# Optimization experiments

Hardware: AMD Instinct MI355X
Metric: run time of the kernel (lower is better)

Reference implementation:

```python
import jax, jax.numpy as jnp
import numpy as np

VOL = 100.0  # cubic volume (100,100,100)


def _forward(x, positions, input_weights, features, output_weights,
             connection_radii, thresholds, n_iterations):
    # clamp positions into the volume (per-axis, min 0.1, max VOL-0.1)
    pos = jnp.clip(positions, 0.1, VOL - 0.1)                      # [N,3]
    radii = jnp.clip(connection_radii, 1.0, 50.0)                  # [N]
    # pairwise Euclidean distances via ||a||^2 + ||b||^2 - 2ab (avoids [N,N,3])
    sq = jnp.sum(pos * pos, axis=1)
    d2 = jnp.maximum(sq[:, None] + sq[None, :] - 2.0 * (pos @ pos.T), 0.0)
    pos_mask = d2 > 0.0
    dist = jnp.where(pos_mask, jnp.sqrt(jnp.where(pos_mask, d2, 1.0)), 0.0)  # [N,N]
    max_r = jnp.max(radii)
    conn_mask = (dist < max_r).astype(dist.dtype)
    atten = jnp.exp(-jnp.minimum(dist / (radii[:, None] + 1e-6), 20.0)) * conn_mask
    # feature similarity (F.normalize uses eps as a clamp-min on the norm)
    fn = features / jnp.maximum(jnp.linalg.norm(features, axis=1, keepdims=True), 1e-6)
    feat_sim = fn @ fn.T                                            # [N,N]
    cw = atten * (0.3 + 0.7 * jnp.clip(feat_sim, -1.0, 1.0))
    cw = cw / (jnp.sum(cw, axis=1, keepdims=True) + 1e-6)           # row-normalized [N,N]
    # spatial input / output gating along x-axis
    xc = jnp.clip(pos[:, 0] / VOL, 0.0, 1.0)                        # [N]
    iw = jnp.exp(-3.0 * xc)
    iw = iw / (jnp.sum(iw) + 1e-6)
    act = (x @ input_weights.T) * iw                                # [B,N]
    for _ in range(n_iterations):
        act = jnp.minimum(jax.nn.relu(act + act @ cw.T - thresholds), 100.0)
    ow = jnp.exp(3.0 * (xc - 1.0))
    ow = ow / (jnp.sum(ow) + 1e-6)
    return (act * ow) @ output_weights                              # [B,out]


def setup_inputs() -> dict:
    key = jax.random.key(0)
    ks = jax.random.split(key, 5)
    N, IN, OUT, FD, B = 8000, 784, 10, 32, 64
    return {
        "x": jax.random.normal(ks[0], (B, IN), jnp.float32),
        "positions": jax.random.uniform(ks[1], (N, 3), jnp.float32) * VOL,
        "input_weights": jax.random.normal(ks[2], (N, IN), jnp.float32) * 0.01,
        "features": jax.random.normal(ks[3], (N, FD), jnp.float32) * 0.1,
        "output_weights": jax.random.normal(ks[4], (N, OUT), jnp.float32) * 0.01,
        "connection_radii": jnp.ones((N,), jnp.float32) * 15.0,
        "thresholds": jnp.zeros((N,), jnp.float32),
        "n_iterations": 2,
    }


def reference(x, positions, input_weights, features, output_weights,
              connection_radii, thresholds, n_iterations):
    return _forward(x, positions, input_weights, features, output_weights,
                    connection_radii, thresholds, n_iterations)
```

## Files before the change

### kernel.cpp

```cpp
#include <hip/hip_runtime.h>
#include <hip/hip_bf16.h>
#include <math.h>

#define VOLF 100.0f
#define FD 32
#define OUT_DIM 10
#define MAXN 320
#define MAX_LAUNCH_ITERS 4
#define KSPLIT 7
#define BM 64
#define BKQ 28
#define SRW 2
#define SRB 8
#define OB 128

__global__ __launch_bounds__(256) void k_pre(
    const float* __restrict__ positions, const float* __restrict__ radii_in,
    const float* __restrict__ features, float* __restrict__ posx4,
    float* __restrict__ radii, float* __restrict__ e_iw, float* __restrict__ e_ow,
    float* __restrict__ fn, float* __restrict__ scal, int N)
{
    int i = blockIdx.x * blockDim.x + threadIdx.x;
    float my_iw = 0.0f, my_ow = 0.0f, my_r = 0.0f;
    if (i < N) {
        float px = fminf(fmaxf(positions[3*i+0], 0.1f), VOLF - 0.1f);
        float py = fminf(fmaxf(positions[3*i+1], 0.1f), VOLF - 0.1f);
        float pz = fminf(fmaxf(positions[3*i+2], 0.1f), VOLF - 0.1f);
        float sq = px*px + py*py + pz*pz;
        posx4[4*i+0] = px; posx4[4*i+1] = py; posx4[4*i+2] = pz; posx4[4*i+3] = sq;
        float r = fminf(fmaxf(radii_in[i], 1.0f), 50.0f);
        radii[i] = r; my_r = r;
        float xc = fminf(fmaxf(px / VOLF, 0.0f), 1.0f);
        my_iw = expf(-3.0f * xc);
        my_ow = expf(3.0f * (xc - 1.0f));
        e_iw[i] = my_iw; e_ow[i] = my_ow;
        float s = 0.0f;
        #pragma unroll
        for (int k = 0; k < FD; k++) { float v = features[(size_t)i*FD + k]; s += v*v; }
        float nrm = fmaxf(sqrtf(s), 1e-6f);
        #pragma unroll
        for (int k = 0; k < FD; k++) fn[(size_t)i*FD + k] = features[(size_t)i*FD + k] / nrm;
    }
    __shared__ float red[256];
    red[threadIdx.x] = my_iw; __syncthreads();
    for (int s = 128; s > 0; s >>= 1) { if (threadIdx.x < s) red[threadIdx.x] += red[threadIdx.x + s]; __syncthreads(); }
    if (threadIdx.x == 0) atomicAdd(&scal[0], red[0]);
    __syncthreads();
    red[threadIdx.x] = my_ow; __syncthreads();
    for (int s = 128; s > 0; s >>= 1) { if (threadIdx.x < s) red[threadIdx.x] += red[threadIdx.x + s]; __syncthreads(); }
    if (threadIdx.x == 0) atomicAdd(&scal[1], red[0]);
    if (i < N) atomicMax((int*)&scal[2], __float_as_int(my_r));
}

__global__ __launch_bounds__(256) void k_xt(const float* __restrict__ x, float* __restrict__ xT,
                                            int B, int IN)
{
    int idx = blockIdx.x * blockDim.x + threadIdx.x;
    if (idx < B * IN) {
        int b = idx / IN, k = idx % IN;
        xT[(size_t)k * B + b] = x[idx];
    }
}

__global__ __launch_bounds__(256) void k_act0(
    const float* __restrict__ xT, const float* __restrict__ Wi,
    float* __restrict__ partial, int N, int IN)
{
    __shared__ float4 xs4[BKQ * 64];
    __shared__ float  wt[BM * 112];
    int t = threadIdx.x;
    int i0 = blockIdx.x * BM;
    int k0 = blockIdx.y * 112;
    #pragma unroll
    for (int fi = t; fi < BM * 28; fi += 256) {
        int row = fi / 28, cq = fi % 28;
        ((float4*)wt)[row * 28 + cq] = *(const float4*)(Wi + (size_t)(i0 + row) * IN + k0 + cq * 4);
    }
    {
        int l = t & 63, q = t >> 6;
        #pragma unroll
        for (int kq = q; kq < BKQ; kq += 4) {
            float4 v;
            v.x = xT[(size_t)(k0 + 4*kq + 0) * 64 + l];
            v.y = xT[(size_t)(k0 + 4*kq + 1) * 64 + l];
            v.z = xT[(size_t)(k0 + 4*kq + 2) * 64 + l];
            v.w = xT[(size_t)(k0 + 4*kq + 3) * 64 + l];
            xs4[kq * 64 + l] = v;
        }
    }
    __syncthreads();
    int wave = t >> 6, lane = t & 63;
    int nbase = wave * 16;
    float acc[16];
    #pragma unroll
    for (int n = 0; n < 16; n++) acc[n] = 0.0f;
    for (int kq = 0; kq < BKQ; kq++) {
        float4 xv = xs4[kq * 64 + lane];
        #pragma unroll
        for (int n = 0; n < 16; n++) {
            float4 w = ((const float4*)(wt + (nbase + n) * 112))[kq];
            acc[n] += w.x * xv.x + w.y * xv.y + w.z * xv.z + w.w * xv.w;
        }
    }
    size_t base = ((size_t)blockIdx.y * N + (i0 + nbase)) * 64 + lane;
    #pragma unroll
    for (int n = 0; n < 16; n++)
        partial[base + (size_t)n * 64] = acc[n];
}

__global__ __launch_bounds__(256) void k_act0_red(
    const float* __restrict__ partial, const float* __restrict__ e_iw,
    const float* __restrict__ scal, float* __restrict__ actA, int N)
{
    int idx = blockIdx.x * 256 + threadIdx.x;
    int i = idx >> 6;
    size_t stride = (size_t)N * 64;
    float s = 0.0f;
    #pragma unroll
    for (int ks = 0; ks < KSPLIT; ks++) s += partial[ks * stride + idx];
    float inv = 1.0f / (scal[0] + 1e-6f);
    actA[idx] = s * (e_iw[i] * inv);
}

__device__ __forceinline__ void scan_body(
    const float4& p, const float4& q, int j, float maxr,
    unsigned long long lmask, int2* __restrict__ ep, size_t base, int& cnt)
{
    float d2 = fmaxf(p.w + q.w - 2.0f*(p.x*q.x + p.y*q.y + p.z*q.z), 0.0f);
    float dist = sqrtf(d2);
    bool hit = dist < maxr;
    unsigned long long m = __ballot(hit);
    if (m) {
        if (hit) {
            int pos = cnt + (int)__popcll(m & lmask);
            if (pos < MAXN) ep[base + pos] = make_int2(j, __float_as_int(dist));
        }
        cnt += (int)__popcll(m);
    }
}

__global__ __launch_bounds__(256) void k_scan(
    const float* __restrict__ posx4, const float* __restrict__ scal,
    int2* __restrict__ ep, int* __restrict__ nbr_cnt, int N)
{
    int wave = threadIdx.x >> 6, lane = threadIdx.x & 63;
    int r0 = blockIdx.x * SRB + wave * SRW;
    float4 p0 = ((const float4*)posx4)[r0];
    float4 p1 = ((const float4*)posx4)[r0 + 1];
    float maxr = __int_as_float(((const int*)scal)[2]);
    unsigned long long lmask = (1ull << lane) - 1ull;
    int c0 = 0, c1 = 0;
    size_t base0 = (size_t)r0 * MAXN, base1 = base0 + MAXN;
    int jb = 0;
    for (; jb + 128 <= N; jb += 128) {
        int j0 = jb + lane, j1 = jb + 64 + lane;
        float4 q0 = ((const float4*)posx4)[j0];
        float4 q1 = ((const float4*)posx4)[j1];
        scan_body(p0, q0, j0, maxr, lmask, ep, base0, c0);
        scan_body(p1, q0, j0, maxr, lmask, ep, base1, c1);
        scan_body(p0, q1, j1, maxr, lmask, ep, base0, c0);
        scan_body(p1, q1, j1, maxr, lmask, ep, base1, c1);
    }
    for (; jb < N; jb += 64) {
        int j0 = jb + lane;
        float4 q0 = ((const float4*)posx4)[j0];
        scan_body(p0, q0, j0, maxr, lmask, ep, base0, c0);
        scan_body(p1, q0, j0, maxr, lmask, ep, base1, c1);
    }
    if (lane == 0) {
        nbr_cnt[r0]     = min(c0, MAXN);
        nbr_cnt[r0 + 1] = min(c1, MAXN);
    }
}

__global__ __launch_bounds__(256) void k_weight(
    const float* __restrict__ fn, const float* __restrict__ radii,
    int2* __restrict__ ep ,
    const int* __restrict__ nbr_cnt, float* __restrict__ rowinv, int N)
{
    int i = blockIdx.x;
    int lane = threadIdx.x & 63;
    int wave = threadIdx.x >> 6;
    int sub = lane & 7;
    int eg  = lane >> 3;
    float4 fni = ((const float4*)(fn + (size_t)i * FD))[sub];
    float inv_ri = 1.0f / (radii[i] + 1e-6f);
    int cnt = nbr_cnt[i];
    float s = 0.0f;
    for (int e0 = wave * 8; e0 < cnt; e0 += 32) {
        int e = e0 + eg;
        bool act = e < cnt;
        int ecl = act ? e : (cnt - 1);
        int2 edge = ep[(size_t)i * MAXN + ecl];
        int j      = edge.x;
        float dist = __int_as_float(edge.y);
        float4 fj = ((const float4*)(fn + (size_t)j * FD))[sub];
        float fs = fni.x*fj.x + fni.y*fj.y + fni.z*fj.z + fni.w*fj.w;
        fs += __shfl_xor(fs, 1, 64);
        fs += __shfl_xor(fs, 2, 64);
        fs += __shfl_xor(fs, 4, 64);
        fs = fminf(fmaxf(fs, -1.0f), 1.0f);
        float w = expf(-fminf(dist * inv_ri, 20.0f)) * (0.3f + 0.7f * fs);
        if (act && sub == 0) {
            ((float*)&ep[(size_t)i * MAXN + e])[1] = w;
            s += w;
        }
    }
    __shared__ float red[256];
    red[threadIdx.x] = s; __syncthreads();
    for (int st = 128; st > 0; st >>= 1) { if (threadIdx.x < st) red[threadIdx.x] += red[threadIdx.x + st]; __syncthreads(); }
    if (threadIdx.x == 0) rowinv[i] = 1.0f / (red[0] + 1e-6f);
}

__global__ __launch_bounds__(256) void k_iter(
    const float* __restrict__ actIn, float* __restrict__ actOut,
    const int2* __restrict__ ep, const int* __restrict__ nbr_cnt,
    const float* __restrict__ rowinv, const float* __restrict__ thr,
    const int* __restrict__ nIterPtr, int iterIdx, int N)
{
    if (iterIdx >= min(*nIterPtr, MAX_LAUNCH_ITERS)) return;
    int i = blockIdx.x;
    int wave = threadIdx.x >> 6, lane = threadIdx.x & 63;
    int cnt = nbr_cnt[i];
    float acc = 0.0f;
    for (int e = wave; e < cnt; e += 4) {
        int2 edge = ep[(size_t)i * MAXN + e];
        acc += actIn[(size_t)edge.x * 64 + lane] * __int_as_float(edge.y);
    }
    __shared__ float redA[4 * 64];
    redA[wave * 64 + lane] = acc;
    __syncthreads();
    if (wave == 0) {
        float tot = redA[lane] + redA[64 + lane] + redA[128 + lane] + redA[192 + lane];
        float v = actIn[(size_t)i * 64 + lane] + tot * rowinv[i] - thr[i];
        v = fminf(fmaxf(v, 0.0f), 100.0f);
        actOut[(size_t)i * 64 + lane] = v;
    }
}

__global__ __launch_bounds__(256) void k_out1(
    const float* __restrict__ actA, const float* __restrict__ actB,
    const int* __restrict__ nIterPtr, const float* __restrict__ e_ow,
    const float* __restrict__ scal, const float* __restrict__ outW,
    float* __restrict__ outPart, int N)
{
    int m = min(*nIterPtr, MAX_LAUNCH_ITERS);
    const float* actF = (m & 1) ? actB : actA;
    int wave = threadIdx.x >> 6, lane = threadIdx.x & 63;
    float inv = 1.0f / (scal[1] + 1e-6f);
    float acc[OUT_DIM];
    #pragma unroll
    for (int o = 0; o < OUT_DIM; o++) acc[o] = 0.0f;
    for (int i = blockIdx.x * 4 + wave; i < N; i += OB * 4) {
        float a = actF[(size_t)i * 64 + lane] * (e_ow[i] * inv);
        const float* wo = outW + (size_t)i * OUT_DIM;
        #pragma unroll
        for (int o = 0; o < OUT_DIM; o++) acc[o] += a * wo[o];
    }
    __shared__ float red[4][OUT_DIM][64];
    #pragma unroll
    for (int o = 0; o < OUT_DIM; o++) red[wave][o][lane] = acc[o];
    __syncthreads();
    if (wave == 0) {
        #pragma unroll
        for (int o = 0; o < OUT_DIM; o++) {
            float s = red[0][o][lane] + red[1][o][lane] + red[2][o][lane] + red[3][o][lane];
            outPart[((size_t)blockIdx.x * OUT_DIM + o) * 64 + lane] = s;
        }
    }
}

__global__ __launch_bounds__(256) void k_out2(
    const float* __restrict__ outPart, float* __restrict__ out)
{
    int t = blockIdx.x * 256 + threadIdx.x;
    if (t >= 64 * OUT_DIM) return;
    int b = t / OUT_DIM, o = t % OUT_DIM;
    float s = 0.0f;
    for (int blk = 0; blk < OB; blk++)
        s += outPart[((size_t)blk * OUT_DIM + o) * 64 + b];
    out[t] = s;
}

extern "C" void kernel_launch(void* const* d_in, const int* in_sizes, int n_in,
                              void* d_out, int out_size, void* d_ws, size_t ws_size,
                              hipStream_t stream)
{
    const float* x        = (const float*)d_in[0];
    const float* positions= (const float*)d_in[1];
    const float* Win      = (const float*)d_in[2];
    const float* features = (const float*)d_in[3];
    const float* Wout     = (const float*)d_in[4];
    const float* radii_in = (const float*)d_in[5];
    const float* thr      = (const float*)d_in[6];
    const int*   nIter    = (const int*)  d_in[7];

    const int N  = in_sizes[5];
    const int IN = in_sizes[2] / N;
    const int B  = in_sizes[0] / IN;
    (void)B;

    float* ws = (float*)d_ws;
    size_t off = 0;
    auto alloc = [&](size_t nfloats) { size_t cur = off; off += (nfloats + 63) & ~(size_t)63; return cur; };
    float* xT      = ws + alloc((size_t)B * IN);
    float* posx4   = ws + alloc((size_t)N * 4);
    float* radii   = ws + alloc(N);
    float* e_iw    = ws + alloc(N);
    float* e_ow    = ws + alloc(N);
    float* rowinv  = ws + alloc(N);
    float* scal    = ws + alloc(4);
    float* outPart = ws + alloc((size_t)OB * OUT_DIM * 64);
    float* fn      = ws + alloc((size_t)N * FD);
    float* actA    = ws + alloc((size_t)N * 64);
    float* actB    = ws + alloc((size_t)N * 64);
    int2*  ep      = (int2*)(ws + alloc((size_t)N * MAXN * 2));
    int*   nbr_cnt = (int*)(ws + alloc(N));
    float* partial = (float*)ep;

    hipMemsetAsync(scal, 0, 4 * sizeof(float), stream);

    k_pre<<<(N + 255) / 256, 256, 0, stream>>>(positions, radii_in, features,
                                               posx4, radii, e_iw, e_ow, fn, scal, N);
    k_xt<<<(B * IN + 255) / 256, 256, 0, stream>>>(x, xT, B, IN);
    k_act0<<<dim3(N / BM, KSPLIT), 256, 0, stream>>>(xT, Win, partial, N, IN);
    k_act0_red<<<(N * 64) / 256, 256, 0, stream>>>(partial, e_iw, scal, actA, N);
    k_scan<<<N / SRB, 256, 0, stream>>>(posx4, scal, ep, nbr_cnt, N);
    k_weight<<<N, 256, 0, stream>>>(fn, radii, ep, nbr_cnt, rowinv, N);

    float* bufs[2] = {actA, actB};
    for (int it = 0; it < MAX_LAUNCH_ITERS; it++) {
        k_iter<<<N, 256, 0, stream>>>(bufs[it & 1], bufs[(it + 1) & 1],
                                      ep, nbr_cnt, rowinv, thr, nIter, it, N);
    }
    k_out1<<<OB, 256, 0, stream>>>(actA, actB, nIter, e_ow, scal, Wout, outPart, N);
    k_out2<<<3, 256, 0, stream>>>(outPart, (float*)d_out);
}
```

Measured before the change: 254.4 us.

## Fuse prep kernels, fold edge weighting into scan, retile input GEMM

Merges the x-transpose kernel into the preprocessing kernel, and folds the per-row edge weighting and row-sum into the neighbour-scan kernel so one wave handles its rows end to end. The input projection GEMM is retiled into a register-blocked outer product (4x16 per thread) with a transposed weight tile in shared memory, K split into 4 blocks and intra-block wave pairs reduced before writing 8 partial slices. This cuts launch count and redundant ep/fn traffic, but leaves fewer threads for the weighting step and adds more partial-sum slices to reduce.

```diff
diff --git a/kernel.cpp b/kernel.cpp
--- a/kernel.cpp
+++ b/kernel.cpp
@@ -7,20 +7,30 @@
 #define OUT_DIM 10
 #define MAXN 320
 #define MAX_LAUNCH_ITERS 4
-#define KSPLIT 7
-#define BM 64
-#define BKQ 28
 #define SRW 2
 #define SRB 8
 #define OB 128
-
-__global__ __launch_bounds__(256) void k_pre(
-    const float* __restrict__ positions, const float* __restrict__ radii_in,
-    const float* __restrict__ features, float* __restrict__ posx4,
+#define CHUNK 28
+#define NCHUNK 7
+#define LDP 68
+#define PS 8
+
+__global__ __launch_bounds__(256) void k_prext(
+    const float* __restrict__ x, const float* __restrict__ positions,
+    const float* __restrict__ radii_in, const float* __restrict__ features,
+    float* __restrict__ xT, float* __restrict__ posx4,
     float* __restrict__ radii, float* __restrict__ e_iw, float* __restrict__ e_ow,
-    float* __restrict__ fn, float* __restrict__ scal, int N)
-{
-    int i = blockIdx.x * blockDim.x + threadIdx.x;
+    float* __restrict__ fn, float* __restrict__ scal, int N, int B, int IN, int nxt)
+{
+    if ((int)blockIdx.x < nxt) {
+        int idx = blockIdx.x * 256 + threadIdx.x;
+        if (idx < B * IN) {
+            int b = idx / IN, k = idx % IN;
+            xT[(size_t)k * B + b] = x[idx];
+        }
+        return;
+    }
+    int i = (blockIdx.x - nxt) * 256 + threadIdx.x;
     float my_iw = 0.0f, my_ow = 0.0f, my_r = 0.0f;
     if (i < N) {
         float px = fminf(fmaxf(positions[3*i+0], 0.1f), VOLF - 0.1f);
@@ -52,60 +62,81 @@
     if (i < N) atomicMax((int*)&scal[2], __float_as_int(my_r));
 }
 
-__global__ __launch_bounds__(256) void k_xt(const float* __restrict__ x, float* __restrict__ xT,
-                                            int B, int IN)
-{
-    int idx = blockIdx.x * blockDim.x + threadIdx.x;
-    if (idx < B * IN) {
-        int b = idx / IN, k = idx % IN;
-        xT[(size_t)k * B + b] = x[idx];
-    }
-}
-
 __global__ __launch_bounds__(256) void k_act0(
     const float* __restrict__ xT, const float* __restrict__ Wi,
     float* __restrict__ partial, int N, int IN)
 {
-    __shared__ float4 xs4[BKQ * 64];
-    __shared__ float  wt[BM * 112];
+    __shared__ float smem[2 * 64 * 68];
+    float* wtT = smem;
     int t = threadIdx.x;
-    int i0 = blockIdx.x * BM;
-    int k0 = blockIdx.y * 112;
-    #pragma unroll
-    for (int fi = t; fi < BM * 28; fi += 256) {
-        int row = fi / 28, cq = fi % 28;
-        ((float4*)wt)[row * 28 + cq] = *(const float4*)(Wi + (size_t)(i0 + row) * IN + k0 + cq * 4);
-    }
-    {
-        int l = t & 63, q = t >> 6;
-        #pragma unroll
-        for (int kq = q; kq < BKQ; kq += 4) {
-            float4 v;
-            v.x = xT[(size_t)(k0 + 4*kq + 0) * 64 + l];
-            v.y = xT[(size_t)(k0 + 4*kq + 1) * 64 + l];
-            v.z = xT[(size_t)(k0 + 4*kq + 2) * 64 + l];
-            v.w = xT[(size_t)(k0 + 4*kq + 3) * 64 + l];
-            xs4[kq * 64 + l] = v;
-        }
-    }
-    __syncthreads();
     int wave = t >> 6, lane = t & 63;
-    int nbase = wave * 16;
-    float acc[16];
-    #pragma unroll
-    for (int n = 0; n < 16; n++) acc[n] = 0.0f;
-    for (int kq = 0; kq < BKQ; kq++) {
-        float4 xv = xs4[kq * 64 + lane];
-        #pragma unroll
-        for (int n = 0; n < 16; n++) {
-            float4 w = ((const float4*)(wt + (nbase + n) * 112))[kq];
-            acc[n] += w.x * xv.x + w.y * xv.y + w.z * xv.z + w.w * xv.w;
-        }
-    }
-    size_t base = ((size_t)blockIdx.y * N + (i0 + nbase)) * 64 + lane;
-    #pragma unroll
-    for (int n = 0; n < 16; n++)
-        partial[base + (size_t)n * 64] = acc[n];
+    int nr = lane >> 2, br = lane & 3;
+    int i0 = blockIdx.x * 64;
+    int kbase = blockIdx.y * 196;
+    float acc[4][16];
+    #pragma unroll
+    for (int a = 0; a < 4; a++)
+        #pragma unroll
+        for (int b = 0; b < 16; b++) acc[a][b] = 0.0f;
+
+    for (int c = 0; c < NCHUNK; c++) {
+        int k0 = kbase + c * CHUNK;
+        __syncthreads();
+        for (int fi = t; fi < 64 * (CHUNK/4); fi += 256) {
+            int n = fi / (CHUNK/4), q = fi % (CHUNK/4);
+            float4 w4 = *(const float4*)(Wi + (size_t)(i0 + n) * IN + k0 + q * 4);
+            wtT[(q*4+0)*LDP + n] = w4.x;
+            wtT[(q*4+1)*LDP + n] = w4.y;
+            wtT[(q*4+2)*LDP + n] = w4.z;
+            wtT[(q*4+3)*LDP + n] = w4.w;
+        }
+        __syncthreads();
+        for (int q = ((wave + c) & 3); q < CHUNK/4; q += 4) {
+            #pragma unroll
+            for (int j = 0; j < 4; j++) {
+                int kl = q*4 + j;
+                float4 a4 = *(const float4*)(&wtT[kl * LDP + nr*4]);
+                const float* xr = xT + (size_t)(k0 + kl) * 64 + br*16;
+                float4 b0 = *(const float4*)(xr + 0);
+                float4 b1 = *(const float4*)(xr + 4);
+                float4 b2 = *(const float4*)(xr + 8);
+                float4 b3 = *(const float4*)(xr + 12);
+                #pragma unroll
+                for (int a = 0; a < 4; a++) {
+                    float av = (a==0) ? a4.x : (a==1) ? a4.y : (a==2) ? a4.z : a4.w;
+                    acc[a][ 0] += av*b0.x; acc[a][ 1] += av*b0.y; acc[a][ 2] += av*b0.z; acc[a][ 3] += av*b0.w;
+                    acc[a][ 4] += av*b1.x; acc[a][ 5] += av*b1.y; acc[a][ 6] += av*b1.z; acc[a][ 7] += av*b1.w;
+                    acc[a][ 8] += av*b2.x; acc[a][ 9] += av*b2.y; acc[a][10] += av*b2.z; acc[a][11] += av*b2.w;
+                    acc[a][12] += av*b3.x; acc[a][13] += av*b3.y; acc[a][14] += av*b3.z; acc[a][15] += av*b3.w;
+                }
+            }
+        }
+    }
+    __syncthreads();
+    float4* sm4 = (float4*)smem;
+    int g = wave >> 1;
+    if (wave & 1) {
+        #pragma unroll
+        for (int a = 0; a < 4; a++)
+            #pragma unroll
+            for (int b4 = 0; b4 < 4; b4++)
+                sm4[(g*16 + a*4 + b4) * 64 + lane] =
+                    make_float4(acc[a][b4*4+0], acc[a][b4*4+1], acc[a][b4*4+2], acc[a][b4*4+3]);
+    }
+    __syncthreads();
+    if (!(wave & 1)) {
+        int slot = blockIdx.y * 2 + g;
+        size_t pbase = ((size_t)slot * N + i0 + nr*4) * 64 + br*16;
+        #pragma unroll
+        for (int a = 0; a < 4; a++)
+            #pragma unroll
+            for (int b4 = 0; b4 < 4; b4++) {
+                float4 o = sm4[(g*16 + a*4 + b4) * 64 + lane];
+                o.x += acc[a][b4*4+0]; o.y += acc[a][b4*4+1];
+                o.z += acc[a][b4*4+2]; o.w += acc[a][b4*4+3];
+                *(float4*)(partial + pbase + (size_t)a * 64 + b4*4) = o;
+            }
+    }
 }
 
 __global__ __launch_bounds__(256) void k_act0_red(
@@ -117,7 +148,7 @@
     size_t stride = (size_t)N * 64;
     float s = 0.0f;
     #pragma unroll
-    for (int ks = 0; ks < KSPLIT; ks++) s += partial[ks * stride + idx];
+    for (int p = 0; p < PS; p++) s += partial[p * stride + idx];
     float inv = 1.0f / (scal[0] + 1e-6f);
     actA[idx] = s * (e_iw[i] * inv);
 }
@@ -141,7 +172,8 @@
 
 __global__ __launch_bounds__(256) void k_scan(
     const float* __restrict__ posx4, const float* __restrict__ scal,
-    int2* __restrict__ ep, int* __restrict__ nbr_cnt, int N)
+    const float* __restrict__ fn, const float* __restrict__ radii,
+    int2* __restrict__ ep, int* __restrict__ nbr_cnt, float* __restrict__ rowinv, int N)
 {
     int wave = threadIdx.x >> 6, lane = threadIdx.x & 63;
     int r0 = blockIdx.x * SRB + wave * SRW;
@@ -171,45 +203,38 @@
         nbr_cnt[r0]     = min(c0, MAXN);
         nbr_cnt[r0 + 1] = min(c1, MAXN);
     }
-}
-
-__global__ __launch_bounds__(256) void k_weight(
-    const float* __restrict__ fn, const float* __restrict__ radii,
-    int2* __restrict__ ep ,
-    const int* __restrict__ nbr_cnt, float* __restrict__ rowinv, int N)
-{
-    int i = blockIdx.x;
-    int lane = threadIdx.x & 63;
-    int wave = threadIdx.x >> 6;
     int sub = lane & 7;
     int eg  = lane >> 3;
-    float4 fni = ((const float4*)(fn + (size_t)i * FD))[sub];
-    float inv_ri = 1.0f / (radii[i] + 1e-6f);
-    int cnt = nbr_cnt[i];
-    float s = 0.0f;
-    for (int e0 = wave * 8; e0 < cnt; e0 += 32) {
-        int e = e0 + eg;
-        bool act = e < cnt;
-        int ecl = act ? e : (cnt - 1);
-        int2 edge = ep[(size_t)i * MAXN + ecl];
-        int j      = edge.x;
-        float dist = __int_as_float(edge.y);
-        float4 fj = ((const float4*)(fn + (size_t)j * FD))[sub];
-        float fs = fni.x*fj.x + fni.y*fj.y + fni.z*fj.z + fni.w*fj.w;
-        fs += __shfl_xor(fs, 1, 64);
-        fs += __shfl_xor(fs, 2, 64);
-        fs += __shfl_xor(fs, 4, 64);
-        fs = fminf(fmaxf(fs, -1.0f), 1.0f);
-        float w = expf(-fminf(dist * inv_ri, 20.0f)) * (0.3f + 0.7f * fs);
-        if (act && sub == 0) {
-            ((float*)&ep[(size_t)i * MAXN + e])[1] = w;
-            s += w;
-        }
-    }
-    __shared__ float red[256];
-    red[threadIdx.x] = s; __syncthreads();
-    for (int st = 128; st > 0; st >>= 1) { if (threadIdx.x < st) red[threadIdx.x] += red[threadIdx.x + st]; __syncthreads(); }
-    if (threadIdx.x == 0) rowinv[i] = 1.0f / (red[0] + 1e-6f);
+    #pragma unroll
+    for (int rr = 0; rr < SRW; rr++) {
+        int r = r0 + rr;
+        int cnt = min(rr == 0 ? c0 : c1, MAXN);
+        size_t base = (size_t)r * MAXN;
+        float4 fni = ((const float4*)(fn + (size_t)r * FD))[sub];
+        float inv_ri = 1.0f / (radii[r] + 1e-6f);
+        float s = 0.0f;
+        for (int e0 = 0; e0 < cnt; e0 += 8) {
+            int e = e0 + eg;
+            bool act = e < cnt;
+            int ecl = act ? e : cnt - 1;
+            int2 edge = ep[base + ecl];
+            float dist = __int_as_float(edge.y);
+            float4 fj = ((const float4*)(fn + (size_t)edge.x * FD))[sub];
+            float fs = fni.x*fj.x + fni.y*fj.y + fni.z*fj.z + fni.w*fj.w;
+            fs += __shfl_xor(fs, 1, 64);
+            fs += __shfl_xor(fs, 2, 64);
+            fs += __shfl_xor(fs, 4, 64);
+            fs = fminf(fmaxf(fs, -1.0f), 1.0f);
+            float w = expf(-fminf(dist * inv_ri, 20.0f)) * (0.3f + 0.7f * fs);
+            if (act && sub == 0) {
+                ((float*)&ep[base + e])[1] = w;
+                s += w;
+            }
+        }
+        s += __shfl_xor(s, 1, 64);  s += __shfl_xor(s, 2, 64);  s += __shfl_xor(s, 4, 64);
+        s += __shfl_xor(s, 8, 64);  s += __shfl_xor(s, 16, 64); s += __shfl_xor(s, 32, 64);
+        if (lane == 0) rowinv[r] = 1.0f / (s + 1e-6f);
+    }
 }
 
 __global__ __launch_bounds__(256) void k_iter(
@@ -298,7 +323,6 @@
     const int N  = in_sizes[5];
     const int IN = in_sizes[2] / N;
     const int B  = in_sizes[0] / IN;
-    (void)B;
 
     float* ws = (float*)d_ws;
     size_t off = 0;
@@ -320,13 +344,14 @@
 
     hipMemsetAsync(scal, 0, 4 * sizeof(float), stream);
 
-    k_pre<<<(N + 255) / 256, 256, 0, stream>>>(positions, radii_in, features,
-                                               posx4, radii, e_iw, e_ow, fn, scal, N);
-    k_xt<<<(B * IN + 255) / 256, 256, 0, stream>>>(x, xT, B, IN);
-    k_act0<<<dim3(N / BM, KSPLIT), 256, 0, stream>>>(xT, Win, partial, N, IN);
+    int nxt = (B * IN + 255) / 256;
+    int npre = (N + 255) / 256;
+    k_prext<<<nxt + npre, 256, 0, stream>>>(x, positions, radii_in, features,
+                                            xT, posx4, radii, e_iw, e_ow, fn, scal,
+                                            N, B, IN, nxt);
+    k_act0<<<dim3(N / 64, 4), 256, 0, stream>>>(xT, Win, partial, N, IN);
     k_act0_red<<<(N * 64) / 256, 256, 0, stream>>>(partial, e_iw, scal, actA, N);
-    k_scan<<<N / SRB, 256, 0, stream>>>(posx4, scal, ep, nbr_cnt, N);
-    k_weight<<<N, 256, 0, stream>>>(fn, radii, ep, nbr_cnt, rowinv, N);
+    k_scan<<<N / SRB, 256, 0, stream>>>(posx4, scal, fn, radii, ep, nbr_cnt, rowinv, N);
 
     float* bufs[2] = {actA, actB};
     for (int it = 0; it < MAX_LAUNCH_ITERS; it++) {
```

Result: slower. 269.0 us (+5.7%).
